# Performance work log

Hardware: AMD Instinct MI355X
Metric: run time of the kernel (lower is better)

## Reference

```python
import jax, jax.numpy as jnp
import numpy as np

V, E, H2, T = 50000, 300, 256, 9  # vocab, emb dim, per-direction hidden, tag set
B, S = 128, 512


def setup_inputs() -> dict:
    key = jax.random.key(0)
    ks = jax.random.split(key, 16)
    sc_e = 1.0 / np.sqrt(H2)
    inp = {
        'char_ids': jax.random.randint(ks[0], (B, S), 0, V),
        'mask': jnp.ones((B, S), dtype=bool),
        'emb_matrix': jax.random.normal(ks[1], (V, E), jnp.float32) * 0.1,
        'w_ih_f': jax.random.uniform(ks[2], (4 * H2, E), jnp.float32, -sc_e, sc_e),
        'w_hh_f': jax.random.uniform(ks[3], (4 * H2, H2), jnp.float32, -sc_e, sc_e),
        'b_ih_f': jax.random.uniform(ks[4], (4 * H2,), jnp.float32, -sc_e, sc_e),
        'b_hh_f': jax.random.uniform(ks[5], (4 * H2,), jnp.float32, -sc_e, sc_e),
        'w_ih_b': jax.random.uniform(ks[6], (4 * H2, E), jnp.float32, -sc_e, sc_e),
        'w_hh_b': jax.random.uniform(ks[7], (4 * H2, H2), jnp.float32, -sc_e, sc_e),
        'b_ih_b': jax.random.uniform(ks[8], (4 * H2,), jnp.float32, -sc_e, sc_e),
        'b_hh_b': jax.random.uniform(ks[9], (4 * H2,), jnp.float32, -sc_e, sc_e),
        'W_out': jax.random.normal(ks[10], (T, 2 * H2), jnp.float32) * 0.02,
        'b_out': jnp.zeros((T,), jnp.float32),
        'start_trans': jax.random.uniform(ks[11], (T,), jnp.float32, -0.1, 0.1),
        'trans': jax.random.uniform(ks[12], (T, T), jnp.float32, -0.1, 0.1),
        'end_trans': jax.random.uniform(ks[13], (T,), jnp.float32, -0.1, 0.1),
    }
    return inp


def _lstm_dir(x, w_ih, w_hh, b_ih, b_hh, reverse):
    # x: [B, S, E]; PyTorch gate order i, f, g, o
    b, s, _ = x.shape
    h = w_hh.shape[1]
    pre = jnp.einsum('bse,ge->bsg', x, w_ih) + b_ih + b_hh  # [B, S, 4H]
    pre = pre.transpose(1, 0, 2)  # [S, B, 4H]

    def step(carry, xt):
        hh, cc = carry
        g = xt + hh @ w_hh.T
        i, f, gg, o = jnp.split(g, 4, axis=-1)
        i = jax.nn.sigmoid(i)
        f = jax.nn.sigmoid(f)
        gg = jnp.tanh(gg)
        o = jax.nn.sigmoid(o)
        cc = f * cc + i * gg
        hh = o * jnp.tanh(cc)
        return (hh, cc), hh

    init = (jnp.zeros((b, h), x.dtype), jnp.zeros((b, h), x.dtype))
    _, ys = jax.lax.scan(step, init, pre, reverse=reverse)
    return ys.transpose(1, 0, 2)  # [B, S, H]


def _viterbi(emissions, mask, start_trans, trans, end_trans):
    # emissions: [B, S, T], mask: [B, S] bool
    b, s, t = emissions.shape
    score0 = start_trans + emissions[:, 0]  # [B, T]
    em = emissions[:, 1:].transpose(1, 0, 2)  # [S-1, B, T]
    mk = mask[:, 1:].T  # [S-1, B]

    def fwd(score, inp):
        em_t, m_t = inp
        nxt = score[:, :, None] + trans[None] + em_t[:, None, :]  # [B, T, T]
        best = nxt.max(axis=1)
        bp = nxt.argmax(axis=1).astype(jnp.int32)  # [B, T]
        return jnp.where(m_t[:, None], best, score), bp

    score, bps = jax.lax.scan(fwd, score0, (em, mk))  # bps: [S-1, B, T]
    final = score + end_trans
    best_score = final.max(axis=-1)  # [B]
    last_tag = final.argmax(axis=-1).astype(jnp.int32)  # [B]

    bidx = jnp.arange(b)

    def back(tag, inp):
        bp_t, m_t = inp
        new = jnp.where(m_t, bp_t[bidx, tag], tag)
        return new, new

    _, tags = jax.lax.scan(back, last_tag, (bps, mk), reverse=True)  # [S-1, B]
    paths = jnp.concatenate([tags, last_tag[None]], axis=0).T  # [B, S]
    return best_score, paths


def reference(char_ids, mask, emb_matrix, w_ih_f, w_hh_f, b_ih_f, b_hh_f,
              w_ih_b, w_hh_b, b_ih_b, b_hh_b, W_out, b_out,
              start_trans, trans, end_trans):
    emb = emb_matrix[char_ids]  # [B, S, E]
    out_f = _lstm_dir(emb, w_ih_f, w_hh_f, b_ih_f, b_hh_f, reverse=False)
    out_b = _lstm_dir(emb, w_ih_b, w_hh_b, b_ih_b, b_hh_b, reverse=True)
    hs = jnp.concatenate([out_f, out_b], axis=-1)  # [B, S, 2*H2]; dropout is identity in eval
    emissions = jnp.einsum('bsh,th->bst', hs, W_out) + b_out  # [B, S, T]
    return _viterbi(emissions, mask, start_trans, trans, end_trans)
```

## Files before the change

### kernel.cpp

```cpp
#include <hip/hip_runtime.h>
#include <stdint.h>

typedef _Float16 half8 __attribute__((ext_vector_type(8)));
typedef _Float16 half4 __attribute__((ext_vector_type(4)));
typedef float f32x4 __attribute__((ext_vector_type(4)));

#define NB 128
#define NS 512
#define NE 300
#define KE 320
#define NH 256
#define NT 9

#define MFMA16(a, b, c) __builtin_amdgcn_mfma_f32_16x16x32_f16((a), (b), (c), 0, 0, 0)

union HU { _Float16 h; unsigned short u; };
union U64H { unsigned long long q[2]; half8 v; };

__device__ inline half8 ld_h8_agent(const _Float16* p) {
  U64H u;
  u.q[0] = __hip_atomic_load((const unsigned long long*)p,
                             __ATOMIC_RELAXED, __HIP_MEMORY_SCOPE_AGENT);
  u.q[1] = __hip_atomic_load(((const unsigned long long*)p) + 1,
                             __ATOMIC_RELAXED, __HIP_MEMORY_SCOPE_AGENT);
  return u.v;
}

__global__ __launch_bounds__(256) void k_gather(const int* __restrict__ cid,
    const float* __restrict__ emb, _Float16* __restrict__ xhi,
    _Float16* __restrict__ xlo) {
  int wid = threadIdx.x >> 6, lane = threadIdx.x & 63;
  int row = blockIdx.x * 4 + wid;
  int s = row >> 7, b = row & 127;
  int c = cid[b * NS + s];
  const float* src = emb + (size_t)c * NE;
  size_t o = (size_t)row * KE;
#pragma unroll
  for (int i = 0; i < 5; ++i) {
    int k = i * 64 + lane;
    float v = (k < NE) ? src[k] : 0.0f;
    _Float16 hi = (_Float16)v;
    _Float16 lo = (_Float16)((v - (float)hi) * 2048.0f);
    xhi[o + k] = hi;
    xlo[o + k] = lo;
  }
}

__global__ __launch_bounds__(256, 1) void k_lstm(
    const _Float16* __restrict__ xhi, const _Float16* __restrict__ xlo,
    _Float16* __restrict__ hhi_g, _Float16* __restrict__ hlo_g,
    uint32_t* __restrict__ flags,
    const float* __restrict__ wih_f, const float* __restrict__ whh_f,
    const float* __restrict__ bih_f, const float* __restrict__ bhh_f,
    const float* __restrict__ wih_b, const float* __restrict__ whh_b,
    const float* __restrict__ bih_b, const float* __restrict__ bhh_b) {
  __shared__ float gl[4][16][20];

  const int tid = threadIdx.x;
  const int wid = tid >> 6, lane = tid & 63;
  const int beta = (int)blockIdx.x;
  const int dir = beta >> 7;
  const int bc  = beta & 7;
  const int bsl = (beta >> 3) & 15;
  const int gid = (dir << 3) | bc;
  const int u0 = bsl * 16, B0 = bc * 16;
  uint32_t* const flbase = flags + gid * 256;
  uint32_t* const myflag = flbase + bsl * 16;

  const float* Wih = dir ? wih_b : wih_f;
  const float* Whh = dir ? whh_b : whh_f;
  const float* Bih = dir ? bih_b : bih_f;
  const float* Bhh = dir ? bhh_b : bhh_f;

  const int col = lane & 15, kb = (lane >> 4) * 8;
  const int grow = wid * NH + u0 + col;
  half8 wxh[10], wxl[10], whh_h[8], whh_l[8];
#pragma unroll
  for (int kc = 0; kc < 10; ++kc) {
    half8 a, b;
#pragma unroll
    for (int j = 0; j < 8; ++j) {
      int k = kc * 32 + kb + j;
      float v = (k < NE) ? Wih[(size_t)grow * NE + k] : 0.0f;
      _Float16 hi = (_Float16)v;
      a[j] = hi;
      b[j] = (_Float16)((v - (float)hi) * 2048.0f);
    }
    wxh[kc] = a; wxl[kc] = b;
  }
#pragma unroll
  for (int kc = 0; kc < 8; ++kc) {
    half8 a, b;
#pragma unroll
    for (int j = 0; j < 8; ++j) {
      int k = kc * 32 + kb + j;
      float v = Whh[(size_t)grow * NH + k];
      _Float16 hi = (_Float16)v;
      a[j] = hi;
      b[j] = (_Float16)((v - (float)hi) * 2048.0f);
    }
    whh_h[kc] = a; whh_l[kc] = b;
  }
#pragma unroll
  for (int kc = 0; kc < 10; ++kc)
    asm volatile("" : "+v"(wxh[kc]), "+v"(wxl[kc]));
#pragma unroll
  for (int kc = 0; kc < 8; ++kc)
    asm volatile("" : "+v"(whh_h[kc]), "+v"(whh_l[kc]));

  const int eb = tid >> 4, eu = tid & 15;
  float bias_r[4];
#pragma unroll
  for (int w = 0; w < 4; ++w)
    bias_r[w] = Bih[w * NH + u0 + eu] + Bhh[w * NH + u0 + eu];
  float c_reg = 0.0f;

  const int ar = lane & 15, ak = (lane >> 4) * 8;
  const int slo = ak >> 4;
  const int uo  = ak & 8;

  half8 xa_h[10], xa_l[10];
  {
    const int s0 = dir ? (NS - 1) : 0;
    size_t xb = ((size_t)s0 * NB + B0 + ar) * KE + ak;
#pragma unroll
    for (int kc = 0; kc < 10; ++kc) {
      xa_h[kc] = *(const half8*)(xhi + xb + kc * 32);
      xa_l[kc] = *(const half8*)(xlo + xb + kc * 32);
    }
  }

  for (int tau = 0; tau < NS; ++tau) {
    const int s = dir ? (NS - 1 - tau) : tau;

    f32x4 acch = {0.f, 0.f, 0.f, 0.f}, accl = {0.f, 0.f, 0.f, 0.f};
#pragma unroll
    for (int kc = 0; kc < 10; ++kc) {
      acch = MFMA16(xa_h[kc], wxh[kc], acch);
      accl = MFMA16(xa_h[kc], wxl[kc], accl);
      accl = MFMA16(xa_l[kc], wxh[kc], accl);
    }
    {
      const int snx = dir ? (s > 0 ? s - 1 : 0) : (s + 1 < NS ? s + 1 : s);
      size_t xb = ((size_t)snx * NB + B0 + ar) * KE + ak;
#pragma unroll
      for (int kc = 0; kc < 10; ++kc) {
        xa_h[kc] = *(const half8*)(xhi + xb + kc * 32);
        xa_l[kc] = *(const half8*)(xlo + xb + kc * 32);
      }
    }
    __builtin_amdgcn_sched_barrier(0);

    if (tau > 0) {
      {
        const uint32_t* pr = flbase + (lane & 15) * 16;
        for (;;) {
          uint32_t v = __hip_atomic_load(pr, __ATOMIC_RELAXED,
                                         __HIP_MEMORY_SCOPE_AGENT);
          if (__all((int)(v >= (uint32_t)tau))) break;
        }
      }
      const int sprev = dir ? (s + 1) : (s - 1);
      const size_t chunk = ((size_t)(dir * NS + sprev) * 8 + bc) * 4096;
      half8 hh[8], hl[8];
#pragma unroll
      for (int kc = 0; kc < 8; ++kc) {
        size_t off = chunk + (size_t)(kc * 2 + slo) * 256 + ar * 16 + uo;
        hh[kc] = ld_h8_agent(hhi_g + off);
        hl[kc] = ld_h8_agent(hlo_g + off);
      }
#pragma unroll
      for (int kc = 0; kc < 8; ++kc) {
        acch = MFMA16(hh[kc], whh_h[kc], acch);
        accl = MFMA16(hh[kc], whh_l[kc], accl);
        accl = MFMA16(hl[kc], whh_h[kc], accl);
      }
    }

#pragma unroll
    for (int i = 0; i < 4; ++i)
      gl[wid][(lane >> 4) * 4 + i][lane & 15] = acch[i] + accl[i] * 0x1p-11f;
    __syncthreads();

    {
      float gi = gl[0][eb][eu] + bias_r[0];
      float gf = gl[1][eb][eu] + bias_r[1];
      float gg = gl[2][eb][eu] + bias_r[2];
      float go = gl[3][eb][eu] + bias_r[3];
      float si = 1.0f / (1.0f + expf(-gi));
      float sf = 1.0f / (1.0f + expf(-gf));
      float so = 1.0f / (1.0f + expf(-go));
      c_reg = sf * c_reg + si * tanhf(gg);
      float hval = so * tanhf(c_reg);
      _Float16 h16 = (_Float16)hval;
      _Float16 l16 = (_Float16)((hval - (float)h16) * 2048.0f);
      HU a, b; a.h = h16; b.h = l16;
      int oth_hi = __shfl_xor((int)a.u, 1);
      int oth_lo = __shfl_xor((int)b.u, 1);
      if ((eu & 1) == 0) {
        size_t ho = (((size_t)(dir * NS + s) * 8 + bc) * 16 + bsl) * 256
                    + eb * 16 + eu;
        uint32_t whi = (uint32_t)a.u | ((uint32_t)(unsigned short)oth_hi << 16);
        uint32_t wlo = (uint32_t)b.u | ((uint32_t)(unsigned short)oth_lo << 16);
        __hip_atomic_store((uint32_t*)(hhi_g + ho), whi, __ATOMIC_RELAXED,
                           __HIP_MEMORY_SCOPE_AGENT);
        __hip_atomic_store((uint32_t*)(hlo_g + ho), wlo, __ATOMIC_RELAXED,
                           __HIP_MEMORY_SCOPE_AGENT);
      }
    }
    __syncthreads();
    if (tid == 0) {
      __hip_atomic_store(myflag, (uint32_t)(tau + 1), __ATOMIC_RELAXED,
                         __HIP_MEMORY_SCOPE_AGENT);
      asm volatile("s_waitcnt vmcnt(0)" ::: "memory");
    }
  }
}

__global__ __launch_bounds__(256) void k_emis(const _Float16* __restrict__ hhi,
    const _Float16* __restrict__ hlo, const float* __restrict__ Wout,
    const float* __restrict__ bout, float* __restrict__ em) {
  __shared__ float wl[NT * 2 * NH];
  for (int i = threadIdx.x; i < NT * 2 * NH; i += 256) wl[i] = Wout[i];
  __syncthreads();
  int wid = threadIdx.x >> 6, lane = threadIdx.x & 63;
  int row = blockIdx.x * 4 + wid;
  int s = row >> 7, b = row & 127;
  size_t o_f = (((size_t)s * 8 + (b >> 4)) * 16 + (lane >> 2)) * 256
               + (size_t)(b & 15) * 16 + (lane & 3) * 4;
  size_t o_b = ((((size_t)NS + s) * 8 + (b >> 4)) * 16 + (lane >> 2)) * 256
               + (size_t)(b & 15) * 16 + (lane & 3) * 4;
  half4 fh = *(const half4*)(hhi + o_f);
  half4 fl4 = *(const half4*)(hlo + o_f);
  half4 bh = *(const half4*)(hhi + o_b);
  half4 bl4 = *(const half4*)(hlo + o_b);
  float vf[4], vb[4];
#pragma unroll
  for (int j = 0; j < 4; ++j) {
    vf[j] = (float)fh[j] + (float)fl4[j] * 0x1p-11f;
    vb[j] = (float)bh[j] + (float)bl4[j] * 0x1p-11f;
  }
#pragma unroll
  for (int t = 0; t < NT; ++t) {
    float p = 0.f;
#pragma unroll
    for (int j = 0; j < 4; ++j)
      p += vf[j] * wl[t * 512 + lane * 4 + j]
         + vb[j] * wl[t * 512 + 256 + lane * 4 + j];
#pragma unroll
    for (int off = 32; off; off >>= 1) p += __shfl_xor(p, off);
    if (lane == 0) em[((size_t)b * NS + s) * NT + t] = p + bout[t];
  }
}

__global__ __launch_bounds__(64) void k_vit(const float* __restrict__ em,
    const float* __restrict__ st, const float* __restrict__ tr,
    const float* __restrict__ et, float* __restrict__ out) {
  __shared__ unsigned char bp[NS - 1][NT];
  int b = blockIdx.x;
  int j = threadIdx.x;
  const float* eb = em + (size_t)b * NS * NT;
  bool act = j < NT;
  float trc[NT];
#pragma unroll
  for (int i = 0; i < NT; ++i) trc[i] = act ? tr[i * NT + j] : 0.0f;
  float score = act ? (st[j] + eb[j]) : -1e30f;
  float e_nxt = act ? eb[NT + j] : 0.0f;
  for (int s = 1; s < NS; ++s) {
    float e = e_nxt;
    if (s + 1 < NS) e_nxt = act ? eb[(size_t)(s + 1) * NT + j] : 0.0f;
    float sc[NT];
#pragma unroll
    for (int i = 0; i < NT; ++i) sc[i] = __shfl(score, i, 64);
    float best = (sc[0] + trc[0]) + e;
    int bi = 0;
#pragma unroll
    for (int i = 1; i < NT; ++i) {
      float v = (sc[i] + trc[i]) + e;
      if (v > best) { best = v; bi = i; }
    }
    if (act) { bp[s - 1][j] = (unsigned char)bi; score = best; }
  }
  float fin = act ? (score + et[j]) : -3e30f;
  float fv[NT];
#pragma unroll
  for (int i = 0; i < NT; ++i) fv[i] = __shfl(fin, i, 64);
  __syncthreads();
  if (j == 0) {
    float best = fv[0]; int tag = 0;
#pragma unroll
    for (int i = 1; i < NT; ++i) if (fv[i] > best) { best = fv[i]; tag = i; }
    out[b] = best;
    float* po = out + NB + (size_t)b * NS;
    po[NS - 1] = (float)tag;
    for (int s = NS - 2; s >= 0; --s) {
      tag = bp[s][tag];
      po[s] = (float)tag;
    }
  }
}

extern "C" void kernel_launch(void* const* d_in, const int* in_sizes, int n_in,
                              void* d_out, int out_size, void* d_ws, size_t ws_size,
                              hipStream_t stream) {
  const int*   cid   = (const int*)d_in[0];
  const float* emb   = (const float*)d_in[2];
  const float* wih_f = (const float*)d_in[3];
  const float* whh_f = (const float*)d_in[4];
  const float* bih_f = (const float*)d_in[5];
  const float* bhh_f = (const float*)d_in[6];
  const float* wih_b = (const float*)d_in[7];
  const float* whh_b = (const float*)d_in[8];
  const float* bih_b = (const float*)d_in[9];
  const float* bhh_b = (const float*)d_in[10];
  const float* Wout  = (const float*)d_in[11];
  const float* bout  = (const float*)d_in[12];
  const float* st    = (const float*)d_in[13];
  const float* tr    = (const float*)d_in[14];
  const float* et    = (const float*)d_in[15];
  float* out = (float*)d_out;

  const size_t xplane = (size_t)NS * NB * KE * sizeof(_Float16);
  const size_t hplane = (size_t)2 * NS * NB * NH * sizeof(_Float16);
  const size_t em_b   = (size_t)NB * NS * NT * 4;
  const size_t fl_b   = (size_t)16 * 16 * 16 * 4;
  const size_t need = 2 * xplane + 2 * hplane + em_b + fl_b;
  if (ws_size < need) {
    hipMemsetAsync(d_out, 0xFF, 512, stream);
    return;
  }
  char* ws = (char*)d_ws;
  _Float16* xhi   = (_Float16*)ws;
  _Float16* xlo   = (_Float16*)(ws + xplane);
  _Float16* hhi   = (_Float16*)(ws + 2 * xplane);
  _Float16* hlo   = (_Float16*)(ws + 2 * xplane + hplane);
  float*    em    = (float*)(ws + 2 * xplane + 2 * hplane);
  uint32_t* flg   = (uint32_t*)(ws + 2 * xplane + 2 * hplane + em_b);

  hipMemsetAsync(flg, 0, fl_b, stream);
  hipLaunchKernelGGL(k_gather, dim3(16384), dim3(256), 0, stream,
                     cid, emb, xhi, xlo);
  hipLaunchKernelGGL(k_lstm, dim3(256), dim3(256), 0, stream, xhi, xlo,
                     hhi, hlo, flg,
                     wih_f, whh_f, bih_f, bhh_f, wih_b, whh_b, bih_b, bhh_b);
  hipLaunchKernelGGL(k_emis, dim3(16384), dim3(256), 0, stream,
                     hhi, hlo, Wout, bout, em);
  hipLaunchKernelGGL(k_vit, dim3(128), dim3(64), 0, stream, em, st, tr, et, out);
}
```

Baseline: 2.504 ms.

## Give each wave all four gates and per-wave flags with progressive polling

Remaps the MFMA output columns so each wave computes all four gates for its own four hidden units. The gate nonlinearity can then read only that wave's LDS region, which removes both per-step __syncthreads. Each wave publishes its own progress flag (flag array enlarged to 64 per group). Consumers poll per 32-unit chunk and start the recurrent MFMAs for a chunk as soon as its producer waves are done, rather than waiting for all blocks first. The cost is more flag traffic and spinning, and the ordering now rests on per-wave vmcnt waits instead of block barriers.

```diff
diff --git a/kernel.cpp b/kernel.cpp
--- a/kernel.cpp
+++ b/kernel.cpp
@@ -54,37 +54,39 @@
     const float* __restrict__ bih_f, const float* __restrict__ bhh_f,
     const float* __restrict__ wih_b, const float* __restrict__ whh_b,
     const float* __restrict__ bih_b, const float* __restrict__ bhh_b) {
-  __shared__ float gl[4][16][20];
+  __shared__ float gl[4][4][16][4];
 
   const int tid = threadIdx.x;
-  const int wid = tid >> 6, lane = tid & 63;
+  const int wid = tid >> 6;
+  const int L   = tid & 63;
   const int beta = (int)blockIdx.x;
   const int dir = beta >> 7;
   const int bc  = beta & 7;
   const int bsl = (beta >> 3) & 15;
   const int gid = (dir << 3) | bc;
   const int u0 = bsl * 16, B0 = bc * 16;
-  uint32_t* const flbase = flags + gid * 256;
-  uint32_t* const myflag = flbase + bsl * 16;
+  uint32_t* const fbase  = flags + (size_t)gid * 1024;
+  uint32_t* const myflag = fbase + (size_t)(bsl * 4 + wid) * 16;
+  const uint32_t* const pollf = fbase + (size_t)L * 16;
 
   const float* Wih = dir ? wih_b : wih_f;
   const float* Whh = dir ? whh_b : whh_f;
   const float* Bih = dir ? bih_b : bih_f;
   const float* Bhh = dir ? bhh_b : bhh_f;
 
-  const int col = lane & 15, kb = (lane >> 4) * 8;
-  const int grow = wid * NH + u0 + col;
+  const int wg = (L & 15) >> 2, wj = L & 3, kb = (L >> 4) * 8;
+  const int grow = wg * NH + u0 + wid * 4 + wj;
   half8 wxh[10], wxl[10], whh_h[8], whh_l[8];
 #pragma unroll
   for (int kc = 0; kc < 10; ++kc) {
     half8 a, b;
 #pragma unroll
-    for (int j = 0; j < 8; ++j) {
-      int k = kc * 32 + kb + j;
+    for (int jj = 0; jj < 8; ++jj) {
+      int k = kc * 32 + kb + jj;
       float v = (k < NE) ? Wih[(size_t)grow * NE + k] : 0.0f;
       _Float16 hi = (_Float16)v;
-      a[j] = hi;
-      b[j] = (_Float16)((v - (float)hi) * 2048.0f);
+      a[jj] = hi;
+      b[jj] = (_Float16)((v - (float)hi) * 2048.0f);
     }
     wxh[kc] = a; wxl[kc] = b;
   }
@@ -92,12 +94,12 @@
   for (int kc = 0; kc < 8; ++kc) {
     half8 a, b;
 #pragma unroll
-    for (int j = 0; j < 8; ++j) {
-      int k = kc * 32 + kb + j;
+    for (int jj = 0; jj < 8; ++jj) {
+      int k = kc * 32 + kb + jj;
       float v = Whh[(size_t)grow * NH + k];
       _Float16 hi = (_Float16)v;
-      a[j] = hi;
-      b[j] = (_Float16)((v - (float)hi) * 2048.0f);
+      a[jj] = hi;
+      b[jj] = (_Float16)((v - (float)hi) * 2048.0f);
     }
     whh_h[kc] = a; whh_l[kc] = b;
   }
@@ -108,14 +110,14 @@
   for (int kc = 0; kc < 8; ++kc)
     asm volatile("" : "+v"(whh_h[kc]), "+v"(whh_l[kc]));
 
-  const int eb = tid >> 4, eu = tid & 15;
+  const int cb = L >> 2, cu = L & 3;
   float bias_r[4];
 #pragma unroll
-  for (int w = 0; w < 4; ++w)
-    bias_r[w] = Bih[w * NH + u0 + eu] + Bhh[w * NH + u0 + eu];
+  for (int g = 0; g < 4; ++g)
+    bias_r[g] = Bih[g * NH + u0 + wid * 4 + cu] + Bhh[g * NH + u0 + wid * 4 + cu];
   float c_reg = 0.0f;
 
-  const int ar = lane & 15, ak = (lane >> 4) * 8;
+  const int ar = L & 15, ak = (L >> 4) * 8;
   const int slo = ak >> 4;
   const int uo  = ak & 8;
 
@@ -152,41 +154,40 @@
     __builtin_amdgcn_sched_barrier(0);
 
     if (tau > 0) {
-      {
-        const uint32_t* pr = flbase + (lane & 15) * 16;
-        for (;;) {
-          uint32_t v = __hip_atomic_load(pr, __ATOMIC_RELAXED,
-                                         __HIP_MEMORY_SCOPE_AGENT);
-          if (__all((int)(v >= (uint32_t)tau))) break;
-        }
-      }
       const int sprev = dir ? (s + 1) : (s - 1);
       const size_t chunk = ((size_t)(dir * NS + sprev) * 8 + bc) * 4096;
-      half8 hh[8], hl[8];
+      bool seen = false;
 #pragma unroll
       for (int kc = 0; kc < 8; ++kc) {
+        const unsigned long long m = 0xFFull << (8 * kc);
+        for (;;) {
+          if (!seen) {
+            uint32_t v = __hip_atomic_load(pollf, __ATOMIC_RELAXED,
+                                           __HIP_MEMORY_SCOPE_AGENT);
+            seen = (v >= (uint32_t)tau);
+          }
+          unsigned long long bal = __ballot((int)seen);
+          if ((bal & m) == m) break;
+        }
+        asm volatile("" ::: "memory");
         size_t off = chunk + (size_t)(kc * 2 + slo) * 256 + ar * 16 + uo;
-        hh[kc] = ld_h8_agent(hhi_g + off);
-        hl[kc] = ld_h8_agent(hlo_g + off);
+        half8 hh = ld_h8_agent(hhi_g + off);
+        half8 hl = ld_h8_agent(hlo_g + off);
+        acch = MFMA16(hh, whh_h[kc], acch);
+        accl = MFMA16(hh, whh_l[kc], accl);
+        accl = MFMA16(hl, whh_h[kc], accl);
       }
-#pragma unroll
-      for (int kc = 0; kc < 8; ++kc) {
-        acch = MFMA16(hh[kc], whh_h[kc], acch);
-        accl = MFMA16(hh[kc], whh_l[kc], accl);
-        accl = MFMA16(hl[kc], whh_h[kc], accl);
-      }
     }
 
 #pragma unroll
     for (int i = 0; i < 4; ++i)
-      gl[wid][(lane >> 4) * 4 + i][lane & 15] = acch[i] + accl[i] * 0x1p-11f;
-    __syncthreads();
+      gl[wid][wg][(L >> 4) * 4 + i][wj] = acch[i] + accl[i] * 0x1p-11f;
+    float gi = gl[wid][0][cb][cu] + bias_r[0];
+    float gf = gl[wid][1][cb][cu] + bias_r[1];
+    float gg = gl[wid][2][cb][cu] + bias_r[2];
+    float go = gl[wid][3][cb][cu] + bias_r[3];
 
     {
-      float gi = gl[0][eb][eu] + bias_r[0];
-      float gf = gl[1][eb][eu] + bias_r[1];
-      float gg = gl[2][eb][eu] + bias_r[2];
-      float go = gl[3][eb][eu] + bias_r[3];
       float si = 1.0f / (1.0f + expf(-gi));
       float sf = 1.0f / (1.0f + expf(-gf));
       float so = 1.0f / (1.0f + expf(-go));
@@ -197,9 +198,9 @@
       HU a, b; a.h = h16; b.h = l16;
       int oth_hi = __shfl_xor((int)a.u, 1);
       int oth_lo = __shfl_xor((int)b.u, 1);
-      if ((eu & 1) == 0) {
+      if ((L & 1) == 0) {
         size_t ho = (((size_t)(dir * NS + s) * 8 + bc) * 16 + bsl) * 256
-                    + eb * 16 + eu;
+                    + cb * 16 + wid * 4 + cu;
         uint32_t whi = (uint32_t)a.u | ((uint32_t)(unsigned short)oth_hi << 16);
         uint32_t wlo = (uint32_t)b.u | ((uint32_t)(unsigned short)oth_lo << 16);
         __hip_atomic_store((uint32_t*)(hhi_g + ho), whi, __ATOMIC_RELAXED,
@@ -208,12 +209,12 @@
                            __HIP_MEMORY_SCOPE_AGENT);
       }
     }
-    __syncthreads();
-    if (tid == 0) {
+    asm volatile("s_waitcnt vmcnt(0)" ::: "memory");
+    if (L == 0) {
       __hip_atomic_store(myflag, (uint32_t)(tau + 1), __ATOMIC_RELAXED,
                          __HIP_MEMORY_SCOPE_AGENT);
-      asm volatile("s_waitcnt vmcnt(0)" ::: "memory");
-    }
+    }
+    asm volatile("s_waitcnt vmcnt(0)" ::: "memory");
   }
 }
 
@@ -323,7 +324,7 @@
   const size_t xplane = (size_t)NS * NB * KE * sizeof(_Float16);
   const size_t hplane = (size_t)2 * NS * NB * NH * sizeof(_Float16);
   const size_t em_b   = (size_t)NB * NS * NT * 4;
-  const size_t fl_b   = (size_t)16 * 16 * 16 * 4;
+  const size_t fl_b   = (size_t)16 * 64 * 16 * 4;
   const size_t need = 2 * xplane + 2 * hplane + em_b + fl_b;
   if (ws_size < need) {
     hipMemsetAsync(d_out, 0xFF, 512, stream);
```

Measured after the change: 3.365 ms. +34.4%, slower.
